# Kernel optimization log

Measured on AMD Instinct MI355X. Metric: run time of the kernel, lower is better.

## Reference

```python
import jax, jax.numpy as jnp
import numpy as np

D_MODEL = 1024
NUM_HEADS = 16
D_K = D_MODEL // NUM_HEADS
B, S = 1, 4096


def setup_inputs() -> dict:
    key = jax.random.key(0)
    ks = jax.random.split(key, 11)
    std = 1.0 / np.sqrt(D_MODEL)
    def lin(k):
        kw, kb = jax.random.split(k)
        W = jax.random.uniform(kw, (D_MODEL, D_MODEL), jnp.float32, -std, std)
        b = jax.random.uniform(kb, (D_MODEL,), jnp.float32, -std, std)
        return W, b
    Wq, bq = lin(ks[0]); Wk, bk = lin(ks[1]); Wv, bv = lin(ks[2]); Wo, bo = lin(ks[3])
    q = jax.random.normal(ks[4], (B, S, D_MODEL), jnp.float32)
    k = jax.random.normal(ks[5], (B, S, D_MODEL), jnp.float32)
    v = jax.random.normal(ks[6], (B, S, D_MODEL), jnp.float32)
    return {"q": q, "k": k, "v": v,
            "Wq": Wq, "bq": bq, "Wk": Wk, "bk": bk,
            "Wv": Wv, "bv": bv, "Wo": Wo, "bo": bo}


def reference(q, k, v, Wq, bq, Wk, bk, Wv, bv, Wo, bo):
    Bq, Sq, _ = q.shape
    # Linear projections (torch Linear: x @ W.T + b)
    def split_heads(x):
        return x.reshape(Bq, -1, NUM_HEADS, D_K).transpose(0, 2, 1, 3)  # [B,H,S,Dk]
    query = split_heads(q @ Wq.T + bq)
    key_ = split_heads(k @ Wk.T + bk)
    value = split_heads(v @ Wv.T + bv)
    scores = jnp.einsum('bhsd,bhtd->bhst', query, key_) / jnp.sqrt(jnp.float32(D_K))
    attn = jax.nn.softmax(scores, axis=-1)  # [B,H,S,S]
    ctx = jnp.einsum('bhst,bhtd->bhsd', attn, value)
    ctx = ctx.transpose(0, 2, 1, 3).reshape(Bq, Sq, NUM_HEADS * D_K)
    return ctx @ Wo.T + bo
```

## Files before the change

### kernel.cpp

```cpp
#include <hip/hip_runtime.h>
#include <cstdint>
#include <cstddef>

#define S_LEN 4096
#define DMODEL 1024
#define NHEADS 16
#define DK 64
#define ACT (S_LEN * DMODEL)
#define WELE (DMODEL * DMODEL)

typedef __bf16 bf16;
typedef bf16  bf16x4 __attribute__((ext_vector_type(4)));
typedef bf16  bf16x8 __attribute__((ext_vector_type(8)));
typedef float f32x4  __attribute__((ext_vector_type(4)));

__device__ __forceinline__ void async16(const void* g, void* l) {
    __builtin_amdgcn_global_load_lds(
        (__attribute__((address_space(1))) void*)(uintptr_t)g,
        (__attribute__((address_space(3))) void*)(uintptr_t)l,
        16, 0, 0);
}

__device__ __forceinline__ float fast_exp2(float x) {
#if __has_builtin(__builtin_amdgcn_exp2f)
    return __builtin_amdgcn_exp2f(x);
#else
    return exp2f(x);
#endif
}

__global__ void __launch_bounds__(256) cvt7(
    const float* a0, const float* a1, const float* a2,
    const float* w0, const float* w1, const float* w2, const float* w3,
    bf16* oa0, bf16* oa1, bf16* oa2,
    bf16* ow0, bf16* ow1, bf16* ow2, bf16* ow3,
    int nA, int nB)
{
    const float* s; bf16* d; int n4;
    switch (blockIdx.y) {
        case 0: s = a0; d = oa0; n4 = nA; break;
        case 1: s = a1; d = oa1; n4 = nA; break;
        case 2: s = a2; d = oa2; n4 = nA; break;
        case 3: s = w0; d = ow0; n4 = nB; break;
        case 4: s = w1; d = ow1; n4 = nB; break;
        case 5: s = w2; d = ow2; n4 = nB; break;
        default: s = w3; d = ow3; n4 = nB; break;
    }
    int i = blockIdx.x * 256 + threadIdx.x;
    if (i < n4) {
        float4 v = ((const float4*)s)[i];
        bf16x4 r = { (bf16)v.x, (bf16)v.y, (bf16)v.z, (bf16)v.w };
        ((bf16x4*)d)[i] = r;
    }
}

__device__ __forceinline__ void gemm_compute_128(
    const bf16* As, const bf16* Bs, f32x4 (&acc)[4][4],
    int wm, int wn, int l16, int quad)
{
    bf16x8 af[4], bfr[4];
#pragma unroll
    for (int i = 0; i < 4; ++i)
        af[i] = *(const bf16x8*)&As[(wm + i * 16 + l16) * 32 + quad * 8];
#pragma unroll
    for (int i = 0; i < 4; ++i)
        bfr[i] = *(const bf16x8*)&Bs[(wn + i * 16 + l16) * 32 + quad * 8];
#pragma unroll
    for (int mi = 0; mi < 4; ++mi)
#pragma unroll
        for (int ni = 0; ni < 4; ++ni)
            acc[mi][ni] = __builtin_amdgcn_mfma_f32_16x16x32_bf16(
                af[mi], bfr[ni], acc[mi][ni], 0, 0, 0);
}

__device__ __forceinline__ void gemm_core_bk64(
    const bf16* __restrict__ A, const bf16* __restrict__ B,
    bf16* As, bf16* Bs, f32x4 (&acc)[4][4],
    int m0, int n0, int wm, int wn, int K)
{
    const int tid  = threadIdx.x;
    const int wave = tid >> 6;
    const int lane = tid & 63;
    const int quad = lane >> 4;
    const int l16  = lane & 15;

    const int srow = tid >> 2;
    const int scol = (tid & 3) * 8;
    const bf16* Ag = A + (size_t)(m0 + srow) * K + scol;
    const bf16* Bg = B + (size_t)(n0 + srow) * K + scol;
    char* lA = (char*)As + wave * 1024;
    char* lB = (char*)Bs + wave * 1024;

    for (int k0 = 0; k0 < K; k0 += 64) {
        async16(Ag,                       lA);
        async16(Ag + (size_t)64 * K,      lA + 4096);
        async16(Ag + 32,                  lA + 8192);
        async16(Ag + 32 + (size_t)64 * K, lA + 12288);
        async16(Bg,                       lB);
        async16(Bg + (size_t)64 * K,      lB + 4096);
        async16(Bg + 32,                  lB + 8192);
        async16(Bg + 32 + (size_t)64 * K, lB + 12288);
        Ag += 64; Bg += 64;
        __syncthreads();

        gemm_compute_128(As,        Bs,        acc, wm, wn, l16, quad);
        gemm_compute_128(As + 4096, Bs + 4096, acc, wm, wn, l16, quad);
        __syncthreads();
    }
}

__global__ void __launch_bounds__(256) proj_qkv(
    const bf16* __restrict__ Xq, const bf16* __restrict__ Wq, const float* __restrict__ bq, bf16* __restrict__ Qo,
    const bf16* __restrict__ Xk, const bf16* __restrict__ Wk, const float* __restrict__ bk, bf16* __restrict__ Ko,
    const bf16* __restrict__ Xv, const bf16* __restrict__ Wv, const float* __restrict__ bv, bf16* __restrict__ Vo,
    float qscale)
{
    __shared__ __align__(16) bf16 As[2 * 128 * 32];
    __shared__ __align__(16) bf16 Bs[2 * 128 * 32];

    const int which = blockIdx.z;
    const bf16*  A    = (which == 0) ? Xq : (which == 1) ? Xk : Xv;
    const bf16*  Bw   = (which == 0) ? Wq : (which == 1) ? Wk : Wv;
    const float* bias = (which == 0) ? bq : (which == 1) ? bk : bv;
    const float  scale = (which == 0) ? qscale : 1.0f;

    const int tid  = threadIdx.x;
    const int wave = tid >> 6;
    const int lane = tid & 63;
    const int quad = lane >> 4;
    const int l16  = lane & 15;
    const int m0 = blockIdx.x * 128;
    const int n0 = blockIdx.y * 128;
    const int wm = (wave & 1) * 64;
    const int wn = (wave >> 1) * 64;

    f32x4 acc[4][4] = {};
    gemm_core_bk64(A, Bw, As, Bs, acc, m0, n0, wm, wn, DMODEL);

    if (which < 2) {
        bf16* out = (which == 0) ? Qo : Ko;
#pragma unroll
        for (int mi = 0; mi < 4; ++mi)
#pragma unroll
            for (int ni = 0; ni < 4; ++ni) {
                const int n = n0 + wn + ni * 16 + l16;
                const float bn = bias[n];
                const int dk = n & 63;
                const int cc = dk >> 3, ee = dk & 7;
                const size_t hb = (size_t)(n >> 6) * S_LEN * DK;
#pragma unroll
                for (int r = 0; r < 4; ++r) {
                    const int m = m0 + wm + mi * 16 + quad * 4 + r;
                    const int pdk = ((cc ^ (m & 7)) << 3) | ee;
                    out[hb + (size_t)m * DK + pdk] = (bf16)((acc[mi][ni][r] + bn) * scale);
                }
            }
    } else {
#pragma unroll
        for (int mi = 0; mi < 4; ++mi)
#pragma unroll
            for (int ni = 0; ni < 4; ++ni) {
                const int n = n0 + wn + ni * 16 + l16;
                const float bn = bias[n];
                const int dk = n & 63;
                const size_t hb = (size_t)(n >> 6) * (64 * S_LEN);
                const int mbase = m0 + wm + mi * 16 + quad * 4;
                const int T  = mbase >> 6;
                const int tt = mbase & 63;
                const int pos = (((tt >> 3) ^ (dk & 7)) << 3) | (tt & 7);
                bf16x4 r4;
#pragma unroll
                for (int r = 0; r < 4; ++r) r4[r] = (bf16)(acc[mi][ni][r] + bn);
                *(bf16x4*)&Vo[hb + (size_t)T * 4096 + dk * 64 + pos] = r4;
            }
    }
}

__global__ void __launch_bounds__(256) gemm_out(
    const bf16* __restrict__ A, const bf16* __restrict__ Bw,
    const float* __restrict__ bias, float* __restrict__ out)
{
    __shared__ __align__(16) bf16 As[64 * 32];
    __shared__ __align__(16) bf16 Bs[128 * 32];

    const int tid  = threadIdx.x;
    const int wave = tid >> 6;
    const int lane = tid & 63;
    const int quad = lane >> 4;
    const int l16  = lane & 15;
    const int m0 = blockIdx.x * 64;
    const int n0 = blockIdx.y * 128;
    const int wm = (wave & 1) * 32;
    const int wn = (wave >> 1) * 64;

    const int srow = tid >> 2;
    const int scol = (tid & 3) * 8;
    const bf16* Ag  = A  + (size_t)(m0 + srow) * DMODEL + scol;
    const bf16* Bg  = Bw + (size_t)(n0 + srow) * DMODEL + scol;
    const bf16* Bg2 = Bg + (size_t)64 * DMODEL;

    f32x4 acc[2][4] = {};
    for (int k0 = 0; k0 < DMODEL; k0 += 32) {
        async16(Ag,  (char*)As + wave * 1024);
        async16(Bg,  (char*)Bs + wave * 1024);
        async16(Bg2, (char*)Bs + 4096 + wave * 1024);
        Ag += 32; Bg += 32; Bg2 += 32;
        __syncthreads();

        bf16x8 af[2], bfr[4];
#pragma unroll
        for (int i = 0; i < 2; ++i)
            af[i] = *(const bf16x8*)&As[(wm + i * 16 + l16) * 32 + quad * 8];
#pragma unroll
        for (int i = 0; i < 4; ++i)
            bfr[i] = *(const bf16x8*)&Bs[(wn + i * 16 + l16) * 32 + quad * 8];

#pragma unroll
        for (int mi = 0; mi < 2; ++mi)
#pragma unroll
            for (int ni = 0; ni < 4; ++ni)
                acc[mi][ni] = __builtin_amdgcn_mfma_f32_16x16x32_bf16(
                    af[mi], bfr[ni], acc[mi][ni], 0, 0, 0);
        __syncthreads();
    }

#pragma unroll
    for (int mi = 0; mi < 2; ++mi)
#pragma unroll
        for (int ni = 0; ni < 4; ++ni) {
            const int n = n0 + wn + ni * 16 + l16;
            const float bn = bias[n];
#pragma unroll
            for (int r = 0; r < 4; ++r) {
                const int m = m0 + wm + mi * 16 + quad * 4 + r;
                out[(size_t)m * DMODEL + n] = acc[mi][ni][r] + bn;
            }
        }
}

__global__ void __launch_bounds__(256) flash_attn(
    const bf16* __restrict__ Q, const bf16* __restrict__ Kh,
    const bf16* __restrict__ Vt, bf16* __restrict__ ctx)
{
    __shared__ __align__(16) bf16 Qs[128 * 64];
    __shared__ __align__(16) bf16 Ks[2][64 * 64];
    __shared__ __align__(16) bf16 Vs[2][64 * 64];
    __shared__ __align__(16) bf16 Ps[4][32 * 68];

    const int tid  = threadIdx.x;
    const int wave = tid >> 6;
    const int lane = tid & 63;
    const int quad = lane >> 4;
    const int l16  = lane & 15;
    const int key8  = (quad ^ (l16 & 7)) << 3;
    const int key8b = key8 ^ 32;
    const int s0 = blockIdx.x * 128;
    const int h  = blockIdx.y;

    const bf16* Kg = Kh + (size_t)h * S_LEN * DK + tid * 8;
    const bf16* Vg = Vt + (size_t)h * (64 * S_LEN) + tid * 8;

    {
        const bf16* Qg = Q + (size_t)h * S_LEN * DK + (size_t)s0 * DK + tid * 8;
#pragma unroll
        for (int j = 0; j < 4; ++j)
            async16(Qg + j * 2048, (char*)Qs + j * 4096 + wave * 1024);
    }
    async16(Kg,        (char*)Ks + wave * 1024);
    async16(Kg + 2048, (char*)Ks + 4096 + wave * 1024);
    async16(Vg,        (char*)Vs + wave * 1024);
    async16(Vg + 2048, (char*)Vs + 4096 + wave * 1024);
    Kg += 4096; Vg += 4096;
    __syncthreads();

    bf16x8 aq[2][2];
#pragma unroll
    for (int mi = 0; mi < 2; ++mi) {
        const bf16* qb = &Qs[(wave * 32 + mi * 16 + l16) * 64];
        aq[mi][0] = *(const bf16x8*)(qb + key8);
        aq[mi][1] = *(const bf16x8*)(qb + key8b);
    }

    f32x4 o[2][4] = {};
    f32x4 lsum4[2] = {};
    bf16* Pw = &Ps[wave][0];
    int cur = 0;

    for (int it = 0; it < 64; ++it) {
        if (it < 63) {
            char* lK = (char*)Ks + (cur ^ 1) * 8192 + wave * 1024;
            char* lV = (char*)Vs + (cur ^ 1) * 8192 + wave * 1024;
            async16(Kg,        lK);
            async16(Kg + 2048, lK + 4096);
            async16(Vg,        lV);
            async16(Vg + 2048, lV + 4096);
            Kg += 4096; Vg += 4096;
        }
        const bf16* Kc = &Ks[cur][0];
        const bf16* Vc = &Vs[cur][0];

        f32x4 sc[2][4] = {};
        __builtin_amdgcn_s_setprio(1);
#pragma unroll
        for (int ti = 0; ti < 4; ++ti) {
            const bf16* kp = &Kc[(ti * 16 + l16) * 64];
            bf16x8 bk0 = *(const bf16x8*)(kp + key8);
            bf16x8 bk1 = *(const bf16x8*)(kp + key8b);
#pragma unroll
            for (int mi = 0; mi < 2; ++mi) {
                sc[mi][ti] = __builtin_amdgcn_mfma_f32_16x16x32_bf16(bk0, aq[mi][0], sc[mi][ti], 0, 0, 0);
                sc[mi][ti] = __builtin_amdgcn_mfma_f32_16x16x32_bf16(bk1, aq[mi][1], sc[mi][ti], 0, 0, 0);
            }
        }
        __builtin_amdgcn_s_setprio(0);

#pragma unroll
        for (int mi = 0; mi < 2; ++mi) {
            const int prow = (mi * 16 + l16) * 68;
#pragma unroll
            for (int ti = 0; ti < 4; ++ti) {
                f32x4 p;
#pragma unroll
                for (int r = 0; r < 4; ++r)
                    p[r] = fast_exp2(sc[mi][ti][r]);
                lsum4[mi] += p;
                bf16x4 pk = { (bf16)p[0], (bf16)p[1], (bf16)p[2], (bf16)p[3] };
                *(bf16x4*)&Pw[prow + ti * 16 + quad * 4] = pk;
            }
        }

        __builtin_amdgcn_s_setprio(1);
#pragma unroll
        for (int mi = 0; mi < 2; ++mi) {
            const bf16* pb = &Pw[(mi * 16 + l16) * 68];
            bf16x4 p0a = *(const bf16x4*)(pb + quad * 8);
            bf16x4 p0b = *(const bf16x4*)(pb + quad * 8 + 4);
            bf16x4 p1a = *(const bf16x4*)(pb + 32 + quad * 8);
            bf16x4 p1b = *(const bf16x4*)(pb + 32 + quad * 8 + 4);
            bf16x8 ap0 = __builtin_shufflevector(p0a, p0b, 0, 1, 2, 3, 4, 5, 6, 7);
            bf16x8 ap1 = __builtin_shufflevector(p1a, p1b, 0, 1, 2, 3, 4, 5, 6, 7);
#pragma unroll
            for (int di = 0; di < 4; ++di) {
                const bf16* vp = &Vc[(di * 16 + l16) * 64];
                bf16x8 bv0 = *(const bf16x8*)(vp + key8);
                bf16x8 bv1 = *(const bf16x8*)(vp + key8b);
                o[mi][di] = __builtin_amdgcn_mfma_f32_16x16x32_bf16(bv0, ap0, o[mi][di], 0, 0, 0);
                o[mi][di] = __builtin_amdgcn_mfma_f32_16x16x32_bf16(bv1, ap1, o[mi][di], 0, 0, 0);
            }
        }
        __builtin_amdgcn_s_setprio(0);

        __syncthreads();
        cur ^= 1;
    }

#pragma unroll
    for (int mi = 0; mi < 2; ++mi) {
        float ls = lsum4[mi][0] + lsum4[mi][1] + lsum4[mi][2] + lsum4[mi][3];
        ls += __shfl_xor(ls, 16);
        ls += __shfl_xor(ls, 32);
        const float rinv = 1.0f / ls;
        const int s = s0 + wave * 32 + mi * 16 + l16;
#pragma unroll
        for (int di = 0; di < 4; ++di) {
            bf16x4 r4 = { (bf16)(o[mi][di][0] * rinv), (bf16)(o[mi][di][1] * rinv),
                          (bf16)(o[mi][di][2] * rinv), (bf16)(o[mi][di][3] * rinv) };
            *(bf16x4*)&ctx[(size_t)s * DMODEL + h * DK + di * 16 + quad * 4] = r4;
        }
    }
}

extern "C" void kernel_launch(void* const* d_in, const int* in_sizes, int n_in,
                              void* d_out, int out_size, void* d_ws, size_t ws_size,
                              hipStream_t stream)
{
    (void)in_sizes; (void)n_in; (void)out_size; (void)ws_size;
    const float* q  = (const float*)d_in[0];
    const float* k  = (const float*)d_in[1];
    const float* v  = (const float*)d_in[2];
    const float* Wq = (const float*)d_in[3];
    const float* bq = (const float*)d_in[4];
    const float* Wk = (const float*)d_in[5];
    const float* bk = (const float*)d_in[6];
    const float* Wv = (const float*)d_in[7];
    const float* bv = (const float*)d_in[8];
    const float* Wo = (const float*)d_in[9];
    const float* bo = (const float*)d_in[10];

    bf16* Xq  = (bf16*)d_ws;
    bf16* Xk  = Xq  + ACT;
    bf16* Xv  = Xk  + ACT;
    bf16* Wqb = Xv  + ACT;
    bf16* Wkb = Wqb + WELE;
    bf16* Wvb = Wkb + WELE;
    bf16* Wob = Wvb + WELE;
    bf16* Qh  = Wob + WELE;
    bf16* Kh  = Qh  + ACT;
    bf16* Vt  = Kh  + ACT;
    bf16* CTX = Vt  + ACT;

    cvt7<<<dim3(ACT / 4 / 256, 7), 256, 0, stream>>>(
        q, k, v, Wq, Wk, Wv, Wo,
        Xq, Xk, Xv, Wqb, Wkb, Wvb, Wob, ACT / 4, WELE / 4);

    const float qscale = 0.125f * 1.4426950408889634f;
    proj_qkv<<<dim3(S_LEN / 128, DMODEL / 128, 3), 256, 0, stream>>>(
        Xq, Wqb, bq, Qh, Xk, Wkb, bk, Kh, Xv, Wvb, bv, Vt, qscale);

    flash_attn<<<dim3(S_LEN / 128, NHEADS), 256, 0, stream>>>(Qh, Kh, Vt, CTX);

    gemm_out<<<dim3(S_LEN / 64, DMODEL / 128), 256, 0, stream>>>(CTX, Wob, bo, (float*)d_out);
}
```

Before: 273.3 us.

## Switch attention to 32x32x16 MFMA and pass P through registers via permlane32 swap

The flash attention inner loop now uses 32x32x16 bf16 MFMA tiles instead of 16x16x32 for both QK^T and PV. The probability tile is packed into bf16 pairs and rearranged across lane halves with v_permlane32_swap, so it feeds the PV MFMA straight from registers and the per-wave LDS P buffer is removed. This drops the LDS write/read round trip and its waits and cuts MFMA instruction count. In exchange it relies on the gfx950 permlane32_swap instruction and on the accumulator layout matching exactly.

```diff
diff --git a/kernel.cpp b/kernel.cpp
--- a/kernel.cpp
+++ b/kernel.cpp
@@ -10,9 +10,12 @@
 #define WELE (DMODEL * DMODEL)
 
 typedef __bf16 bf16;
+typedef bf16  bf16x2 __attribute__((ext_vector_type(2)));
 typedef bf16  bf16x4 __attribute__((ext_vector_type(4)));
 typedef bf16  bf16x8 __attribute__((ext_vector_type(8)));
 typedef float f32x4  __attribute__((ext_vector_type(4)));
+typedef float f32x16 __attribute__((ext_vector_type(16)));
+typedef unsigned int uint32x4v __attribute__((ext_vector_type(4)));
 
 __device__ __forceinline__ void async16(const void* g, void* l) {
     __builtin_amdgcn_global_load_lds(
@@ -27,6 +30,20 @@
 #else
     return exp2f(x);
 #endif
+}
+
+__device__ __forceinline__ unsigned pk2(float a, float b) {
+    bf16x2 t; t[0] = (bf16)a; t[1] = (bf16)b;
+    return __builtin_bit_cast(unsigned, t);
+}
+
+__device__ __forceinline__ void pl32swap(unsigned &a, unsigned &b) {
+    asm volatile("v_permlane32_swap_b32 %0, %1" : "+v"(a), "+v"(b));
+}
+
+__device__ __forceinline__ bf16x8 mkfrag(unsigned w0, unsigned w1, unsigned w2, unsigned w3) {
+    uint32x4v u = { w0, w1, w2, w3 };
+    return __builtin_bit_cast(bf16x8, u);
 }
 
 __global__ void __launch_bounds__(256) cvt7(
@@ -245,15 +262,13 @@
     __shared__ __align__(16) bf16 Qs[128 * 64];
     __shared__ __align__(16) bf16 Ks[2][64 * 64];
     __shared__ __align__(16) bf16 Vs[2][64 * 64];
-    __shared__ __align__(16) bf16 Ps[4][32 * 68];
 
     const int tid  = threadIdx.x;
     const int wave = tid >> 6;
     const int lane = tid & 63;
-    const int quad = lane >> 4;
-    const int l16  = lane & 15;
-    const int key8  = (quad ^ (l16 & 7)) << 3;
-    const int key8b = key8 ^ 32;
+    const int l31  = lane & 31;
+    const int hi   = lane >> 5;
+    const int x7   = lane & 7;
     const int s0 = blockIdx.x * 128;
     const int h  = blockIdx.y;
 
@@ -273,17 +288,16 @@
     Kg += 4096; Vg += 4096;
     __syncthreads();
 
-    bf16x8 aq[2][2];
-#pragma unroll
-    for (int mi = 0; mi < 2; ++mi) {
-        const bf16* qb = &Qs[(wave * 32 + mi * 16 + l16) * 64];
-        aq[mi][0] = *(const bf16x8*)(qb + key8);
-        aq[mi][1] = *(const bf16x8*)(qb + key8b);
-    }
-
-    f32x4 o[2][4] = {};
-    f32x4 lsum4[2] = {};
-    bf16* Pw = &Ps[wave][0];
+    bf16x8 qf[4];
+    {
+        const bf16* qb = &Qs[(wave * 32 + l31) * 64];
+#pragma unroll
+        for (int ks = 0; ks < 4; ++ks)
+            qf[ks] = *(const bf16x8*)(qb + ((((ks << 1) + hi) ^ x7) << 3));
+    }
+
+    f32x16 od[2] = {};
+    float lsum = 0.0f;
     int cur = 0;
 
     for (int it = 0; it < 64; ++it) {
@@ -299,53 +313,49 @@
         const bf16* Kc = &Ks[cur][0];
         const bf16* Vc = &Vs[cur][0];
 
-        f32x4 sc[2][4] = {};
+        f32x16 st[2] = {};
         __builtin_amdgcn_s_setprio(1);
 #pragma unroll
-        for (int ti = 0; ti < 4; ++ti) {
-            const bf16* kp = &Kc[(ti * 16 + l16) * 64];
-            bf16x8 bk0 = *(const bf16x8*)(kp + key8);
-            bf16x8 bk1 = *(const bf16x8*)(kp + key8b);
-#pragma unroll
-            for (int mi = 0; mi < 2; ++mi) {
-                sc[mi][ti] = __builtin_amdgcn_mfma_f32_16x16x32_bf16(bk0, aq[mi][0], sc[mi][ti], 0, 0, 0);
-                sc[mi][ti] = __builtin_amdgcn_mfma_f32_16x16x32_bf16(bk1, aq[mi][1], sc[mi][ti], 0, 0, 0);
+        for (int tt = 0; tt < 2; ++tt) {
+            const bf16* kb = &Kc[(tt * 32 + l31) * 64];
+#pragma unroll
+            for (int ks = 0; ks < 4; ++ks) {
+                bf16x8 kf = *(const bf16x8*)(kb + ((((ks << 1) + hi) ^ x7) << 3));
+                st[tt] = __builtin_amdgcn_mfma_f32_32x32x16_bf16(kf, qf[ks], st[tt], 0, 0, 0);
             }
         }
         __builtin_amdgcn_s_setprio(0);
 
-#pragma unroll
-        for (int mi = 0; mi < 2; ++mi) {
-            const int prow = (mi * 16 + l16) * 68;
-#pragma unroll
-            for (int ti = 0; ti < 4; ++ti) {
-                f32x4 p;
-#pragma unroll
-                for (int r = 0; r < 4; ++r)
-                    p[r] = fast_exp2(sc[mi][ti][r]);
-                lsum4[mi] += p;
-                bf16x4 pk = { (bf16)p[0], (bf16)p[1], (bf16)p[2], (bf16)p[3] };
-                *(bf16x4*)&Pw[prow + ti * 16 + quad * 4] = pk;
+        bf16x8 pf[4];
+#pragma unroll
+        for (int tt = 0; tt < 2; ++tt) {
+            float p[16];
+#pragma unroll
+            for (int r = 0; r < 16; ++r) {
+                p[r] = fast_exp2(st[tt][r]);
+                lsum += p[r];
+            }
+#pragma unroll
+            for (int w = 0; w < 2; ++w) {
+                const int G = w * 8;
+                unsigned A0 = pk2(p[G + 0], p[G + 1]);
+                unsigned A1 = pk2(p[G + 2], p[G + 3]);
+                unsigned B0 = pk2(p[G + 4], p[G + 5]);
+                unsigned B1 = pk2(p[G + 6], p[G + 7]);
+                pl32swap(A0, B0);
+                pl32swap(A1, B1);
+                pf[tt * 2 + w] = mkfrag(A0, A1, B0, B1);
             }
         }
 
         __builtin_amdgcn_s_setprio(1);
 #pragma unroll
-        for (int mi = 0; mi < 2; ++mi) {
-            const bf16* pb = &Pw[(mi * 16 + l16) * 68];
-            bf16x4 p0a = *(const bf16x4*)(pb + quad * 8);
-            bf16x4 p0b = *(const bf16x4*)(pb + quad * 8 + 4);
-            bf16x4 p1a = *(const bf16x4*)(pb + 32 + quad * 8);
-            bf16x4 p1b = *(const bf16x4*)(pb + 32 + quad * 8 + 4);
-            bf16x8 ap0 = __builtin_shufflevector(p0a, p0b, 0, 1, 2, 3, 4, 5, 6, 7);
-            bf16x8 ap1 = __builtin_shufflevector(p1a, p1b, 0, 1, 2, 3, 4, 5, 6, 7);
-#pragma unroll
-            for (int di = 0; di < 4; ++di) {
-                const bf16* vp = &Vc[(di * 16 + l16) * 64];
-                bf16x8 bv0 = *(const bf16x8*)(vp + key8);
-                bf16x8 bv1 = *(const bf16x8*)(vp + key8b);
-                o[mi][di] = __builtin_amdgcn_mfma_f32_16x16x32_bf16(bv0, ap0, o[mi][di], 0, 0, 0);
-                o[mi][di] = __builtin_amdgcn_mfma_f32_16x16x32_bf16(bv1, ap1, o[mi][di], 0, 0, 0);
+        for (int dd = 0; dd < 2; ++dd) {
+            const bf16* vb = &Vc[(dd * 32 + l31) * 64];
+#pragma unroll
+            for (int ks = 0; ks < 4; ++ks) {
+                bf16x8 vf = *(const bf16x8*)(vb + ((((ks << 1) + hi) ^ x7) << 3));
+                od[dd] = __builtin_amdgcn_mfma_f32_32x32x16_bf16(vf, pf[ks], od[dd], 0, 0, 0);
             }
         }
         __builtin_amdgcn_s_setprio(0);
@@ -354,20 +364,19 @@
         cur ^= 1;
     }
 
-#pragma unroll
-    for (int mi = 0; mi < 2; ++mi) {
-        float ls = lsum4[mi][0] + lsum4[mi][1] + lsum4[mi][2] + lsum4[mi][3];
-        ls += __shfl_xor(ls, 16);
-        ls += __shfl_xor(ls, 32);
-        const float rinv = 1.0f / ls;
-        const int s = s0 + wave * 32 + mi * 16 + l16;
-#pragma unroll
-        for (int di = 0; di < 4; ++di) {
-            bf16x4 r4 = { (bf16)(o[mi][di][0] * rinv), (bf16)(o[mi][di][1] * rinv),
-                          (bf16)(o[mi][di][2] * rinv), (bf16)(o[mi][di][3] * rinv) };
-            *(bf16x4*)&ctx[(size_t)s * DMODEL + h * DK + di * 16 + quad * 4] = r4;
-        }
-    }
+    lsum += __shfl_xor(lsum, 32);
+    const float rinv = 1.0f / lsum;
+    const int s = s0 + wave * 32 + l31;
+#pragma unroll
+    for (int dd = 0; dd < 2; ++dd)
+#pragma unroll
+        for (int g = 0; g < 4; ++g) {
+            bf16x4 r4;
+#pragma unroll
+            for (int r = 0; r < 4; ++r)
+                r4[r] = (bf16)(od[dd][g * 4 + r] * rinv);
+            *(bf16x4*)&ctx[(size_t)s * DMODEL + h * DK + dd * 32 + g * 8 + hi * 4] = r4;
+        }
 }
 
 extern "C" void kernel_launch(void* const* d_in, const int* in_sizes, int n_in,
```

Result: no change. 269.0 us (-1.6%).
